# Performance work log

Hardware: AMD Instinct MI355X
Metric: run time of the kernel (lower is better)

## Reference

```python
import jax, jax.numpy as jnp
import numpy as np

B, H, S, D = 2, 16, 2048, 128

def setup_inputs() -> dict:
    key = jax.random.key(0)
    kq, kk, kv = jax.random.split(key, 3)
    queries = jax.random.normal(kq, (B, H, S, D), dtype=jnp.float32)
    keys = jax.random.normal(kk, (B, H, S, D), dtype=jnp.float32)
    values = jax.random.normal(kv, (B, H, S, D), dtype=jnp.float32)
    # causal mask: 1 where future position should be masked out (added * -1e9)
    mask = jnp.triu(jnp.ones((S, S), dtype=jnp.float32), k=1)[None, None]  # [1,1,S,S]
    return {"queries": queries, "keys": keys, "values": values, "mask": mask}

def reference(queries, keys, values, mask):
    d_k = jnp.asarray(keys.shape[-1], dtype=jnp.float32)
    # [B,H,Sq,Sk] attention scores
    scores = jnp.einsum('bhqd,bhkd->bhqk', queries, keys) / jnp.sqrt(d_k)
    scores = scores + mask * (-1e9)
    weights = jax.nn.softmax(scores, axis=-1)
    out = jnp.einsum('bhqk,bhkd->bhqd', weights, values)
    return out
```

## Files before the change

### kernel.cpp

```cpp
#include <hip/hip_runtime.h>

#define S_LEN 2048
#define D_DIM 128

typedef float f4 __attribute__((ext_vector_type(4)));
typedef __bf16 y8 __attribute__((ext_vector_type(8)));
typedef short s4v __attribute__((ext_vector_type(4)));

union Frag {
  unsigned u[4];
  unsigned short h[8];
  y8 v;
};

__device__ __forceinline__ unsigned short f2bf(float f) {
  unsigned u = __float_as_uint(f);
  return (unsigned short)((u + 0x7fffu + ((u >> 16) & 1u)) >> 16);
}

__global__ __launch_bounds__(256, 4) void fattn_kernel(
    const float* __restrict__ Qg0, const float* __restrict__ Kg0,
    const float* __restrict__ Vg0, float* __restrict__ Og0) {
  __shared__ __align__(16) unsigned short kbuf[32 * 128];
  __shared__ __align__(16) unsigned short vtbuf[128 * 40];

  const int qb  = blockIdx.x;
  const int bh  = blockIdx.y;
  const int tid = threadIdx.x;
  const int w   = tid >> 6;
  const int l   = tid & 63;
  const int g   = l >> 4;
  const int qi  = l & 15;

  const int wq    = qb * 64 + w * 16;
  const int q_abs = wq + qi;

  const size_t base = (size_t)bh * S_LEN * D_DIM;
  const float* Qg = Qg0 + base;
  const float* Kg = Kg0 + base;
  const float* Vg = Vg0 + base;
  float*       Og = Og0 + base;

  Frag qf[4];
  {
    const float sc = 0.08838834764831845f;
    const float* qrow = Qg + (size_t)q_abs * D_DIM + g * 8;
#pragma unroll
    for (int c = 0; c < 4; ++c) {
      float4 f0 = *(const float4*)(qrow + c * 32);
      float4 f1 = *(const float4*)(qrow + c * 32 + 4);
      qf[c].h[0] = f2bf(f0.x * sc); qf[c].h[1] = f2bf(f0.y * sc);
      qf[c].h[2] = f2bf(f0.z * sc); qf[c].h[3] = f2bf(f0.w * sc);
      qf[c].h[4] = f2bf(f1.x * sc); qf[c].h[5] = f2bf(f1.y * sc);
      qf[c].h[6] = f2bf(f1.z * sc); qf[c].h[7] = f2bf(f1.w * sc);
    }
  }

  f4 acc[8];
#pragma unroll
  for (int i = 0; i < 8; ++i) acc[i] = (f4){0.f, 0.f, 0.f, 0.f};
  float m_run = -3.0e38f;
  float l_run = 0.f;

  const int nkt = 2 * qb + 2;

  const int sk  = tid >> 3;
  const int sc8 = tid & 7;
  const int sd4 = tid & 31;
  const int skp = tid >> 5;

  for (int kt = 0; kt < nkt; ++kt) {
    const int kb = kt * 32;
    __syncthreads();

#pragma unroll
    for (int p = 0; p < 2; ++p) {
      const int col8 = p * 8 + sc8;
      const float* src = Kg + (size_t)(kb + sk) * D_DIM + col8 * 8;
      float4 f0 = *(const float4*)src;
      float4 f1 = *(const float4*)(src + 4);
      Frag t;
      t.h[0] = f2bf(f0.x); t.h[1] = f2bf(f0.y); t.h[2] = f2bf(f0.z); t.h[3] = f2bf(f0.w);
      t.h[4] = f2bf(f1.x); t.h[5] = f2bf(f1.y); t.h[6] = f2bf(f1.z); t.h[7] = f2bf(f1.w);
      const int so = (col8 * 8) ^ ((sk & 7) << 3);
      *(y8*)&kbuf[sk * 128 + so] = t.v;
    }

    {
      const int k0 = skp * 4, d0 = sd4 * 4;
      const float* vsrc = Vg + (size_t)(kb + k0) * D_DIM + d0;
      float4 r0 = *(const float4*)(vsrc);
      float4 r1 = *(const float4*)(vsrc + D_DIM);
      float4 r2 = *(const float4*)(vsrc + 2 * D_DIM);
      float4 r3 = *(const float4*)(vsrc + 3 * D_DIM);
      *(s4v*)&vtbuf[(d0 + 0) * 40 + k0] =
          (s4v){(short)f2bf(r0.x), (short)f2bf(r1.x), (short)f2bf(r2.x), (short)f2bf(r3.x)};
      *(s4v*)&vtbuf[(d0 + 1) * 40 + k0] =
          (s4v){(short)f2bf(r0.y), (short)f2bf(r1.y), (short)f2bf(r2.y), (short)f2bf(r3.y)};
      *(s4v*)&vtbuf[(d0 + 2) * 40 + k0] =
          (s4v){(short)f2bf(r0.z), (short)f2bf(r1.z), (short)f2bf(r2.z), (short)f2bf(r3.z)};
      *(s4v*)&vtbuf[(d0 + 3) * 40 + k0] =
          (s4v){(short)f2bf(r0.w), (short)f2bf(r1.w), (short)f2bf(r2.w), (short)f2bf(r3.w)};
    }
    __syncthreads();

    if (kb > wq) continue;

    f4 s0 = (f4){0.f, 0.f, 0.f, 0.f};
    f4 s1 = (f4){0.f, 0.f, 0.f, 0.f};
#pragma unroll
    for (int c = 0; c < 4; ++c) {
      const int so = (c * 32 + g * 8) ^ ((qi & 7) << 3);
      y8 a0 = *(const y8*)&kbuf[qi * 128 + so];
      y8 a1 = *(const y8*)&kbuf[(qi + 16) * 128 + so];
      s0 = __builtin_amdgcn_mfma_f32_16x16x32_bf16(a0, qf[c].v, s0, 0, 0, 0);
      s1 = __builtin_amdgcn_mfma_f32_16x16x32_bf16(a1, qf[c].v, s1, 0, 0, 0);
    }

    if (kb + 31 > wq) {
      const int kl = kb + g * 4;
#pragma unroll
      for (int r = 0; r < 4; ++r) {
        if (kl + r > q_abs)      s0[r] = -3.0e38f;
        if (kl + 16 + r > q_abs) s1[r] = -3.0e38f;
      }
    }

    float tmax = fmaxf(fmaxf(fmaxf(s0[0], s0[1]), fmaxf(s0[2], s0[3])),
                       fmaxf(fmaxf(s1[0], s1[1]), fmaxf(s1[2], s1[3])));
    tmax = fmaxf(tmax, __shfl_xor(tmax, 16));
    tmax = fmaxf(tmax, __shfl_xor(tmax, 32));
    const float mnew = fmaxf(m_run, tmax);
    const float scl  = __expf(m_run - mnew);
    float p0 = __expf(s0[0] - mnew), p1 = __expf(s0[1] - mnew);
    float p2 = __expf(s0[2] - mnew), p3 = __expf(s0[3] - mnew);
    float p4 = __expf(s1[0] - mnew), p5 = __expf(s1[1] - mnew);
    float p6 = __expf(s1[2] - mnew), p7 = __expf(s1[3] - mnew);
    float rs = ((p0 + p1) + (p2 + p3)) + ((p4 + p5) + (p6 + p7));
    rs += __shfl_xor(rs, 16);
    rs += __shfl_xor(rs, 32);
    l_run = l_run * scl + rs;
    m_run = mnew;

    f4 srv;
    srv[0] = __shfl(scl, g * 4 + 0);
    srv[1] = __shfl(scl, g * 4 + 1);
    srv[2] = __shfl(scl, g * 4 + 2);
    srv[3] = __shfl(scl, g * 4 + 3);
#pragma unroll
    for (int ch = 0; ch < 8; ++ch) acc[ch] *= srv;

    const unsigned w0 = (unsigned)f2bf(p0) | ((unsigned)f2bf(p1) << 16);
    const unsigned w1 = (unsigned)f2bf(p2) | ((unsigned)f2bf(p3) << 16);
    const unsigned w2 = (unsigned)f2bf(p4) | ((unsigned)f2bf(p5) << 16);
    const unsigned w3 = (unsigned)f2bf(p6) | ((unsigned)f2bf(p7) << 16);
    const int  bs = ((l >> 4) & 1) * 32 + qi;
    const bool hi = (l >= 32);
    unsigned t0  = __shfl(w0, bs),      t2  = __shfl(w2, bs);
    unsigned t1  = __shfl(w1, bs),      t3  = __shfl(w3, bs);
    unsigned t0b = __shfl(w0, bs + 16), t2b = __shfl(w2, bs + 16);
    unsigned t1b = __shfl(w1, bs + 16), t3b = __shfl(w3, bs + 16);
    Frag pa;
    pa.u[0] = hi ? t2  : t0;
    pa.u[1] = hi ? t3  : t1;
    pa.u[2] = hi ? t2b : t0b;
    pa.u[3] = hi ? t3b : t1b;

#pragma unroll
    for (int ch = 0; ch < 8; ++ch) {
      y8 bv = *(const y8*)&vtbuf[(ch * 16 + qi) * 40 + g * 8];
      acc[ch] = __builtin_amdgcn_mfma_f32_16x16x32_bf16(pa.v, bv, acc[ch], 0, 0, 0);
    }
  }

  f4 li;
  li[0] = 1.0f / __shfl(l_run, g * 4 + 0);
  li[1] = 1.0f / __shfl(l_run, g * 4 + 1);
  li[2] = 1.0f / __shfl(l_run, g * 4 + 2);
  li[3] = 1.0f / __shfl(l_run, g * 4 + 3);
#pragma unroll
  for (int ch = 0; ch < 8; ++ch) {
#pragma unroll
    for (int r = 0; r < 4; ++r) {
      Og[(size_t)(wq + g * 4 + r) * D_DIM + ch * 16 + qi] = acc[ch][r] * li[r];
    }
  }
}

extern "C" void kernel_launch(void* const* d_in, const int* in_sizes, int n_in,
                              void* d_out, int out_size, void* d_ws, size_t ws_size,
                              hipStream_t stream) {
  const float* Q = (const float*)d_in[0];
  const float* K = (const float*)d_in[1];
  const float* V = (const float*)d_in[2];
  float* O = (float*)d_out;
  dim3 grid(S_LEN / 64, 32);
  fattn_kernel<<<grid, 256, 0, stream>>>(Q, K, V, O);
}
```

Baseline: 327.8 us.

## Double-buffer 64-key K/V tiles and schedule heavy causal blocks first

Key and value tiles grow from 32 to 64 rows and are double-buffered in LDS, so the next tile is staged while the current one is computed, with one barrier per tile instead of two. The V-transpose buffer switches from padding to an XOR swizzle. Query blocks are launched in reverse order so the longest causal rows start first. Launch bounds drop from 4 to 2 blocks per CU to allow the larger LDS footprint, which risks lower occupancy and more register pressure.

```diff
diff --git a/kernel.cpp b/kernel.cpp
--- a/kernel.cpp
+++ b/kernel.cpp
@@ -18,13 +18,13 @@
   return (unsigned short)((u + 0x7fffu + ((u >> 16) & 1u)) >> 16);
 }
 
-__global__ __launch_bounds__(256, 4) void fattn_kernel(
+__global__ __launch_bounds__(256, 2) void fattn_kernel(
     const float* __restrict__ Qg0, const float* __restrict__ Kg0,
     const float* __restrict__ Vg0, float* __restrict__ Og0) {
-  __shared__ __align__(16) unsigned short kbuf[32 * 128];
-  __shared__ __align__(16) unsigned short vtbuf[128 * 40];
-
-  const int qb  = blockIdx.x;
+  __shared__ __align__(16) unsigned short kbuf[2][64 * 128];
+  __shared__ __align__(16) unsigned short vtbuf[2][128 * 64];
+
+  const int qb  = 31 - (int)blockIdx.x;
   const int bh  = blockIdx.y;
   const int tid = threadIdx.x;
   const int w   = tid >> 6;
@@ -35,7 +35,7 @@
   const int wq    = qb * 64 + w * 16;
   const int q_abs = wq + qi;
 
-  const size_t base = (size_t)bh * S_LEN * D_DIM;
+  const size_t base = (size_t)bh * (S_LEN * D_DIM);
   const float* Qg = Qg0 + base;
   const float* Kg = Kg0 + base;
   const float* Vg = Vg0 + base;
@@ -62,115 +62,129 @@
   float m_run = -3.0e38f;
   float l_run = 0.f;
 
-  const int nkt = 2 * qb + 2;
-
-  const int sk  = tid >> 3;
-  const int sc8 = tid & 7;
-  const int sd4 = tid & 31;
-  const int skp = tid >> 5;
-
-  for (int kt = 0; kt < nkt; ++kt) {
-    const int kb = kt * 32;
-    __syncthreads();
-
-#pragma unroll
-    for (int p = 0; p < 2; ++p) {
-      const int col8 = p * 8 + sc8;
-      const float* src = Kg + (size_t)(kb + sk) * D_DIM + col8 * 8;
+  const int nt = qb + 1;
+
+  auto stage = [&](int tt, int b) {
+    const int kb = tt * 64;
+#pragma unroll
+    for (int it = 0; it < 4; ++it) {
+      const int chunk = it * 256 + tid;
+      const int kk = chunk >> 4;
+      const int c8 = chunk & 15;
+      const float* src = Kg + (size_t)(kb + kk) * D_DIM + c8 * 8;
       float4 f0 = *(const float4*)src;
       float4 f1 = *(const float4*)(src + 4);
-      Frag t;
-      t.h[0] = f2bf(f0.x); t.h[1] = f2bf(f0.y); t.h[2] = f2bf(f0.z); t.h[3] = f2bf(f0.w);
-      t.h[4] = f2bf(f1.x); t.h[5] = f2bf(f1.y); t.h[6] = f2bf(f1.z); t.h[7] = f2bf(f1.w);
-      const int so = (col8 * 8) ^ ((sk & 7) << 3);
-      *(y8*)&kbuf[sk * 128 + so] = t.v;
-    }
-
-    {
-      const int k0 = skp * 4, d0 = sd4 * 4;
+      Frag t2;
+      t2.h[0] = f2bf(f0.x); t2.h[1] = f2bf(f0.y); t2.h[2] = f2bf(f0.z); t2.h[3] = f2bf(f0.w);
+      t2.h[4] = f2bf(f1.x); t2.h[5] = f2bf(f1.y); t2.h[6] = f2bf(f1.z); t2.h[7] = f2bf(f1.w);
+      *(y8*)&kbuf[b][kk * 128 + ((c8 * 8) ^ ((kk & 7) << 3))] = t2.v;
+    }
+#pragma unroll
+    for (int it = 0; it < 2; ++it) {
+      const int bid = it * 256 + tid;
+      const int d0 = (bid & 31) * 4;
+      const int k0 = (bid >> 5) * 4;
       const float* vsrc = Vg + (size_t)(kb + k0) * D_DIM + d0;
       float4 r0 = *(const float4*)(vsrc);
       float4 r1 = *(const float4*)(vsrc + D_DIM);
       float4 r2 = *(const float4*)(vsrc + 2 * D_DIM);
       float4 r3 = *(const float4*)(vsrc + 3 * D_DIM);
-      *(s4v*)&vtbuf[(d0 + 0) * 40 + k0] =
+      *(s4v*)&vtbuf[b][(d0 + 0) * 64 + (k0 ^ (((d0 + 0) & 7) << 3))] =
           (s4v){(short)f2bf(r0.x), (short)f2bf(r1.x), (short)f2bf(r2.x), (short)f2bf(r3.x)};
-      *(s4v*)&vtbuf[(d0 + 1) * 40 + k0] =
+      *(s4v*)&vtbuf[b][(d0 + 1) * 64 + (k0 ^ (((d0 + 1) & 7) << 3))] =
           (s4v){(short)f2bf(r0.y), (short)f2bf(r1.y), (short)f2bf(r2.y), (short)f2bf(r3.y)};
-      *(s4v*)&vtbuf[(d0 + 2) * 40 + k0] =
+      *(s4v*)&vtbuf[b][(d0 + 2) * 64 + (k0 ^ (((d0 + 2) & 7) << 3))] =
           (s4v){(short)f2bf(r0.z), (short)f2bf(r1.z), (short)f2bf(r2.z), (short)f2bf(r3.z)};
-      *(s4v*)&vtbuf[(d0 + 3) * 40 + k0] =
+      *(s4v*)&vtbuf[b][(d0 + 3) * 64 + (k0 ^ (((d0 + 3) & 7) << 3))] =
           (s4v){(short)f2bf(r0.w), (short)f2bf(r1.w), (short)f2bf(r2.w), (short)f2bf(r3.w)};
     }
+  };
+
+  stage(0, 0);
+  __syncthreads();
+  int cur = 0;
+
+  for (int t = 0; t < nt; ++t) {
+    if (t + 1 < nt) stage(t + 1, cur ^ 1);
+
+    const int kb = t * 64;
+    const unsigned short* kp = kbuf[cur];
+    const unsigned short* vp = vtbuf[cur];
+
+#pragma unroll
+    for (int s = 0; s < 2; ++s) {
+      const int kbs = kb + 32 * s;
+      if (kbs > wq + 15) continue;
+
+      f4 s0 = (f4){0.f, 0.f, 0.f, 0.f};
+      f4 s1 = (f4){0.f, 0.f, 0.f, 0.f};
+#pragma unroll
+      for (int c = 0; c < 4; ++c) {
+        const int so = (c * 32 + g * 8) ^ ((qi & 7) << 3);
+        y8 a0 = *(const y8*)&kp[(32 * s + qi) * 128 + so];
+        y8 a1 = *(const y8*)&kp[(32 * s + qi + 16) * 128 + so];
+        s0 = __builtin_amdgcn_mfma_f32_16x16x32_bf16(a0, qf[c].v, s0, 0, 0, 0);
+        s1 = __builtin_amdgcn_mfma_f32_16x16x32_bf16(a1, qf[c].v, s1, 0, 0, 0);
+      }
+
+      if (kbs + 31 > wq) {
+        const int kl = kbs + g * 4;
+#pragma unroll
+        for (int r = 0; r < 4; ++r) {
+          if (kl + r > q_abs)      s0[r] = -3.0e38f;
+          if (kl + 16 + r > q_abs) s1[r] = -3.0e38f;
+        }
+      }
+
+      float tmax = fmaxf(fmaxf(fmaxf(s0[0], s0[1]), fmaxf(s0[2], s0[3])),
+                         fmaxf(fmaxf(s1[0], s1[1]), fmaxf(s1[2], s1[3])));
+      tmax = fmaxf(tmax, __shfl_xor(tmax, 16));
+      tmax = fmaxf(tmax, __shfl_xor(tmax, 32));
+      const float mnew = fmaxf(m_run, tmax);
+      const float scl  = __expf(m_run - mnew);
+      float p0 = __expf(s0[0] - mnew), p1 = __expf(s0[1] - mnew);
+      float p2 = __expf(s0[2] - mnew), p3 = __expf(s0[3] - mnew);
+      float p4 = __expf(s1[0] - mnew), p5 = __expf(s1[1] - mnew);
+      float p6 = __expf(s1[2] - mnew), p7 = __expf(s1[3] - mnew);
+      float rs = ((p0 + p1) + (p2 + p3)) + ((p4 + p5) + (p6 + p7));
+      rs += __shfl_xor(rs, 16);
+      rs += __shfl_xor(rs, 32);
+      l_run = l_run * scl + rs;
+      m_run = mnew;
+
+      f4 srv;
+      srv[0] = __shfl(scl, g * 4 + 0);
+      srv[1] = __shfl(scl, g * 4 + 1);
+      srv[2] = __shfl(scl, g * 4 + 2);
+      srv[3] = __shfl(scl, g * 4 + 3);
+#pragma unroll
+      for (int ch = 0; ch < 8; ++ch) acc[ch] *= srv;
+
+      const unsigned w0 = (unsigned)f2bf(p0) | ((unsigned)f2bf(p1) << 16);
+      const unsigned w1 = (unsigned)f2bf(p2) | ((unsigned)f2bf(p3) << 16);
+      const unsigned w2 = (unsigned)f2bf(p4) | ((unsigned)f2bf(p5) << 16);
+      const unsigned w3 = (unsigned)f2bf(p6) | ((unsigned)f2bf(p7) << 16);
+      const int  bs = ((l >> 4) & 1) * 32 + qi;
+      const bool hb = (l >= 32);
+      unsigned t0  = __shfl(w0, bs),      t2  = __shfl(w2, bs);
+      unsigned t1  = __shfl(w1, bs),      t3  = __shfl(w3, bs);
+      unsigned t0b = __shfl(w0, bs + 16), t2b = __shfl(w2, bs + 16);
+      unsigned t1b = __shfl(w1, bs + 16), t3b = __shfl(w3, bs + 16);
+      Frag pa;
+      pa.u[0] = hb ? t2  : t0;
+      pa.u[1] = hb ? t3  : t1;
+      pa.u[2] = hb ? t2b : t0b;
+      pa.u[3] = hb ? t3b : t1b;
+
+#pragma unroll
+      for (int ch = 0; ch < 8; ++ch) {
+        y8 bv = *(const y8*)&vp[(ch * 16 + qi) * 64 + ((32 * s + g * 8) ^ ((qi & 7) << 3))];
+        acc[ch] = __builtin_amdgcn_mfma_f32_16x16x32_bf16(pa.v, bv, acc[ch], 0, 0, 0);
+      }
+    }
+
     __syncthreads();
-
-    if (kb > wq) continue;
-
-    f4 s0 = (f4){0.f, 0.f, 0.f, 0.f};
-    f4 s1 = (f4){0.f, 0.f, 0.f, 0.f};
-#pragma unroll
-    for (int c = 0; c < 4; ++c) {
-      const int so = (c * 32 + g * 8) ^ ((qi & 7) << 3);
-      y8 a0 = *(const y8*)&kbuf[qi * 128 + so];
-      y8 a1 = *(const y8*)&kbuf[(qi + 16) * 128 + so];
-      s0 = __builtin_amdgcn_mfma_f32_16x16x32_bf16(a0, qf[c].v, s0, 0, 0, 0);
-      s1 = __builtin_amdgcn_mfma_f32_16x16x32_bf16(a1, qf[c].v, s1, 0, 0, 0);
-    }
-
-    if (kb + 31 > wq) {
-      const int kl = kb + g * 4;
-#pragma unroll
-      for (int r = 0; r < 4; ++r) {
-        if (kl + r > q_abs)      s0[r] = -3.0e38f;
-        if (kl + 16 + r > q_abs) s1[r] = -3.0e38f;
-      }
-    }
-
-    float tmax = fmaxf(fmaxf(fmaxf(s0[0], s0[1]), fmaxf(s0[2], s0[3])),
-                       fmaxf(fmaxf(s1[0], s1[1]), fmaxf(s1[2], s1[3])));
-    tmax = fmaxf(tmax, __shfl_xor(tmax, 16));
-    tmax = fmaxf(tmax, __shfl_xor(tmax, 32));
-    const float mnew = fmaxf(m_run, tmax);
-    const float scl  = __expf(m_run - mnew);
-    float p0 = __expf(s0[0] - mnew), p1 = __expf(s0[1] - mnew);
-    float p2 = __expf(s0[2] - mnew), p3 = __expf(s0[3] - mnew);
-    float p4 = __expf(s1[0] - mnew), p5 = __expf(s1[1] - mnew);
-    float p6 = __expf(s1[2] - mnew), p7 = __expf(s1[3] - mnew);
-    float rs = ((p0 + p1) + (p2 + p3)) + ((p4 + p5) + (p6 + p7));
-    rs += __shfl_xor(rs, 16);
-    rs += __shfl_xor(rs, 32);
-    l_run = l_run * scl + rs;
-    m_run = mnew;
-
-    f4 srv;
-    srv[0] = __shfl(scl, g * 4 + 0);
-    srv[1] = __shfl(scl, g * 4 + 1);
-    srv[2] = __shfl(scl, g * 4 + 2);
-    srv[3] = __shfl(scl, g * 4 + 3);
-#pragma unroll
-    for (int ch = 0; ch < 8; ++ch) acc[ch] *= srv;
-
-    const unsigned w0 = (unsigned)f2bf(p0) | ((unsigned)f2bf(p1) << 16);
-    const unsigned w1 = (unsigned)f2bf(p2) | ((unsigned)f2bf(p3) << 16);
-    const unsigned w2 = (unsigned)f2bf(p4) | ((unsigned)f2bf(p5) << 16);
-    const unsigned w3 = (unsigned)f2bf(p6) | ((unsigned)f2bf(p7) << 16);
-    const int  bs = ((l >> 4) & 1) * 32 + qi;
-    const bool hi = (l >= 32);
-    unsigned t0  = __shfl(w0, bs),      t2  = __shfl(w2, bs);
-    unsigned t1  = __shfl(w1, bs),      t3  = __shfl(w3, bs);
-    unsigned t0b = __shfl(w0, bs + 16), t2b = __shfl(w2, bs + 16);
-    unsigned t1b = __shfl(w1, bs + 16), t3b = __shfl(w3, bs + 16);
-    Frag pa;
-    pa.u[0] = hi ? t2  : t0;
-    pa.u[1] = hi ? t3  : t1;
-    pa.u[2] = hi ? t2b : t0b;
-    pa.u[3] = hi ? t3b : t1b;
-
-#pragma unroll
-    for (int ch = 0; ch < 8; ++ch) {
-      y8 bv = *(const y8*)&vtbuf[(ch * 16 + qi) * 40 + g * 8];
-      acc[ch] = __builtin_amdgcn_mfma_f32_16x16x32_bf16(pa.v, bv, acc[ch], 0, 0, 0);
-    }
+    cur ^= 1;
   }
 
   f4 li;
```

After: 346.3 us. 1.06x slower.
